# Kernel tuning notes

Hardware: AMD Instinct MI355X
Metric: run time of the kernel (lower is better)

## Reference

```python
import jax, jax.numpy as jnp
from jax import lax
import numpy as np

BLANK = 0
NEG = -1e30  # finite stand-in for -inf to keep gradients well-defined


def setup_inputs() -> dict:
    key = jax.random.key(0)
    k1, k2, k3, k4 = jax.random.split(key, 4)
    B, T, U, V = 16, 200, 100, 512
    acts = jax.random.normal(k1, (B, T, U + 1, V), dtype=jnp.float32)
    labels = jax.random.randint(k2, (B, U), 1, V, dtype=jnp.int32)  # non-blank labels
    act_lens = jax.random.randint(k3, (B,), 150, T + 1, dtype=jnp.int32)
    label_lens = jax.random.randint(k4, (B,), 50, U + 1, dtype=jnp.int32)
    return {"acts": acts, "labels": labels, "act_lens": act_lens, "label_lens": label_lens}


def _rnnt_costs(acts, labels, act_lens, label_lens):
    """Per-utterance RNN-T negative log-likelihood via forward DP over the
    (time, label) lattice. acts: (B,T,U+1,V) raw logits."""
    B, T, U1, V = acts.shape
    lp = jax.nn.log_softmax(acts, axis=-1)          # (B,T,U1,V)
    blank_lp = lp[..., BLANK]                        # (B,T,U1)
    # emit_lp[b,t,u] = lp[b,t,u,labels[b,u]]; pad labels to U1 (last col masked)
    labels_pad = jnp.pad(labels, ((0, 0), (0, 1)))   # (B,U1)
    idx = jnp.broadcast_to(labels_pad[:, None, :, None], (B, T, U1, 1))
    emit_lp = jnp.take_along_axis(lp, idx, axis=-1)[..., 0]  # (B,T,U1)
    # disallow emitting beyond each utterance's label length
    valid_u = jnp.arange(U1)[None, :] < label_lens[:, None]   # (B,U1)
    emit_lp = jnp.where(valid_u[:, None, :], emit_lp, NEG)

    # alpha[t,u]: log-prob of emitting first u labels using t frames
    # row t=0: alpha[0,u] = sum_{k<u} emit[0,k]
    row0 = jnp.concatenate(
        [jnp.zeros((B, 1), acts.dtype), jnp.cumsum(emit_lp[:, 0, :-1], axis=1)], axis=1)

    def t_step(prev_row, xs):
        blank_tm1, emit_t = xs                       # each (B,U1)
        noemit = prev_row + blank_tm1                # came from (t-1,u) via blank
        a0 = noemit[:, 0]

        def u_step(a_prev, xs_u):
            ne_u, em_um1 = xs_u                      # (B,), (B,)
            a_new = jnp.logaddexp(ne_u, a_prev + em_um1)
            return a_new, a_new

        _, rest = lax.scan(u_step, a0, (noemit[:, 1:].T, emit_t[:, :-1].T))  # (U1-1,B)
        row = jnp.concatenate([a0[:, None], rest.T], axis=1)  # (B,U1)
        return row, row

    xs = (jnp.moveaxis(blank_lp[:, :-1], 1, 0),      # blank at t-1, t=1..T-1
          jnp.moveaxis(emit_lp[:, 1:], 1, 0))        # emit at t,    t=1..T-1
    _, rows = lax.scan(t_step, row0, xs)             # (T-1,B,U1)
    alpha = jnp.concatenate([row0[None], rows], axis=0)  # (T,B,U1)
    alpha = jnp.moveaxis(alpha, 0, 1)                # (B,T,U1)

    b_idx = jnp.arange(B)
    t_idx = act_lens - 1
    u_idx = label_lens
    ll = alpha[b_idx, t_idx, u_idx] + blank_lp[b_idx, t_idx, u_idx]
    return -ll                                       # (B,)


def reference(acts, labels, act_lens, label_lens):
    costs = _rnnt_costs(acts, labels, act_lens, label_lens)
    B = acts.shape[0]
    # reduction='mean' in this impl: sum over batch then divide by batch size
    return (jnp.sum(costs) / B)[None]                # shape (1,)
```

## Files before the change

kernel.cpp:

```cpp
#include <hip/hip_runtime.h>
#include <math.h>

#define NEG -1e30f

constexpr int B  = 16;
constexpr int T  = 200;
constexpr int U  = 100;
constexpr int U1 = 101;
constexpr int V  = 512;
constexpr int NDIAG = T + U1 - 1;

__device__ __forceinline__ float logaddexpf_(float a, float b) {
    float mx = fmaxf(a, b);
    float mn = fminf(a, b);
    return mx + log1pf(__expf(mn - mx));
}

__global__ void lse_extract_kernel(const float* __restrict__ acts,
                                   const int*   __restrict__ labels,
                                   const int*   __restrict__ label_lens,
                                   float* __restrict__ blankD,
                                   float* __restrict__ emitD) {
    const int nrows = B * T * U1;
    int gid   = blockIdx.x * blockDim.x + threadIdx.x;
    int wave  = gid >> 6;
    int lane  = threadIdx.x & 63;
    int nwaves = (gridDim.x * blockDim.x) >> 6;
    for (int row = wave; row < nrows; row += nwaves) {
        const float*  p  = acts + (size_t)row * V;
        const float4* p4 = (const float4*)p;
        float4 x0 = p4[lane * 2];
        float4 x1 = p4[lane * 2 + 1];
        float m = fmaxf(fmaxf(fmaxf(x0.x, x0.y), fmaxf(x0.z, x0.w)),
                        fmaxf(fmaxf(x1.x, x1.y), fmaxf(x1.z, x1.w)));
        #pragma unroll
        for (int off = 32; off; off >>= 1) m = fmaxf(m, __shfl_xor(m, off, 64));
        float s = __expf(x0.x - m) + __expf(x0.y - m) + __expf(x0.z - m) + __expf(x0.w - m)
                + __expf(x1.x - m) + __expf(x1.y - m) + __expf(x1.z - m) + __expf(x1.w - m);
        #pragma unroll
        for (int off = 32; off; off >>= 1) s += __shfl_xor(s, off, 64);
        float lse = m + __logf(s);
        if (lane == 0) {
            int u  = row % U1;
            int bt = row / U1;
            int t  = bt % T;
            int b  = bt / T;
            size_t dpos = ((size_t)b * NDIAG + (t + u)) * U1 + u;
            blankD[dpos] = x0.x - lse;
            float e = NEG;
            if (u < label_lens[b]) {
                int lab = labels[b * U + u];
                e = p[lab] - lse;
            }
            emitD[dpos] = e;
        }
    }
}

__global__ void __launch_bounds__(128) dp_kernel(const float* __restrict__ blankD,
                                                 const float* __restrict__ emitD,
                                                 const int*   __restrict__ act_lens,
                                                 const int*   __restrict__ label_lens,
                                                 float* __restrict__ costs) {
    int b = blockIdx.x;
    int u = threadIdx.x;
    const float* bl = blankD + (size_t)b * NDIAG * U1;
    const float* em = emitD  + (size_t)b * NDIAG * U1;
    int t_end = act_lens[b] - 1;
    int u_end = label_lens[b];
    __shared__ float diag[2][U1];
    if (u == 0) diag[0][0] = 0.0f;
    float bl_r = 0.0f, em_r = 0.0f;
    if (u < U1) {
        bl_r = bl[u];
        if (u >= 1) em_r = em[u - 1];
    }
    __syncthreads();
    for (int d = 1; d < NDIAG; ++d) {
        const float* prev = diag[(d - 1) & 1];
        float*       cur  = diag[d & 1];
        int  t = d - u;
        bool active = (u < U1) && (t >= 0) && (t < T);
        float val = 0.0f;
        if (active) {
            if (t == 0)            val = prev[u - 1] + em_r;
            else if (u == 0)       val = prev[0] + bl_r;
            else                   val = logaddexpf_(prev[u] + bl_r,
                                                     prev[u - 1] + em_r);
        }
        float bl_n = 0.0f, em_n = 0.0f;
        if (u < U1 && d < NDIAG - 1) {
            bl_n = bl[d * U1 + u];
            if (u >= 1) em_n = em[d * U1 + u - 1];
        }
        if (active) {
            cur[u] = val;
            if (t == t_end && u == u_end)
                costs[b] = -(val + bl[d * U1 + u]);
        }
        bl_r = bl_n;
        em_r = em_n;
        __syncthreads();
    }
}

__global__ void finalize_kernel(const float* __restrict__ costs, float* __restrict__ out) {
    int lane = threadIdx.x;
    float v = (lane < B) ? costs[lane] : 0.0f;
    #pragma unroll
    for (int off = 8; off; off >>= 1) v += __shfl_xor(v, off, 64);
    if (lane == 0) out[0] = v * (1.0f / (float)B);
}

extern "C" void kernel_launch(void* const* d_in, const int* in_sizes, int n_in,
                              void* d_out, int out_size, void* d_ws, size_t ws_size,
                              hipStream_t stream) {
    const float* acts       = (const float*)d_in[0];
    const int*   labels     = (const int*)d_in[1];
    const int*   act_lens   = (const int*)d_in[2];
    const int*   label_lens = (const int*)d_in[3];
    float* out = (float*)d_out;

    float* blankD = (float*)d_ws;
    float* emitD  = blankD + (size_t)B * NDIAG * U1;
    float* costs  = emitD  + (size_t)B * NDIAG * U1;

    lse_extract_kernel<<<4096, 256, 0, stream>>>(acts, labels, label_lens, blankD, emitD);
    dp_kernel<<<B, 128, 0, stream>>>(blankD, emitD, act_lens, label_lens, costs);
    finalize_kernel<<<1, 64, 0, stream>>>(costs, out);
}
```

Measured before the change: 1.068 ms.

## Skip lattice rows beyond sequence lengths and run DP in one wave

The log-softmax extraction kernel now skips rows where t is at or past act_len or u is past label_len, writing NEG sentinels instead of reading the 512-wide logits row. This avoids reading and reducing acts that cannot affect the final cost. The diagonal DP kernel is rewritten to use a single 64-lane wave in which each lane holds two lattice cells. Neighbour values are passed with shuffles instead of shared memory and block barriers, and the blank/emit loads are prefetched four diagonals ahead in registers. The result relies on the skipped cells never feeding the cell read at (act_len-1, label_len).

New measurement: 1.084 ms. Within noise of the previous version (+1.5%).

```diff
diff --git a/kernel.cpp b/kernel.cpp
--- a/kernel.cpp
+++ b/kernel.cpp
@@ -18,6 +18,7 @@
 
 __global__ void lse_extract_kernel(const float* __restrict__ acts,
                                    const int*   __restrict__ labels,
+                                   const int*   __restrict__ act_lens,
                                    const int*   __restrict__ label_lens,
                                    float* __restrict__ blankD,
                                    float* __restrict__ emitD) {
@@ -26,7 +27,20 @@
     int wave  = gid >> 6;
     int lane  = threadIdx.x & 63;
     int nwaves = (gridDim.x * blockDim.x) >> 6;
+    int al_v = (lane < B) ? act_lens[lane]   : 0;
+    int ll_v = (lane < B) ? label_lens[lane] : 0;
     for (int row = wave; row < nrows; row += nwaves) {
+        int u  = row % U1;
+        int bt = row / U1;
+        int t  = bt % T;
+        int b  = bt / T;
+        int al = __shfl(al_v, b, 64);
+        int ll = __shfl(ll_v, b, 64);
+        size_t dpos = ((size_t)b * NDIAG + (t + u)) * U1 + u;
+        if (t >= al || u > ll) {
+            if (lane == 0) { blankD[dpos] = NEG; emitD[dpos] = NEG; }
+            continue;
+        }
         const float*  p  = acts + (size_t)row * V;
         const float4* p4 = (const float4*)p;
         float4 x0 = p4[lane * 2];
@@ -41,14 +55,9 @@
         for (int off = 32; off; off >>= 1) s += __shfl_xor(s, off, 64);
         float lse = m + __logf(s);
         if (lane == 0) {
-            int u  = row % U1;
-            int bt = row / U1;
-            int t  = bt % T;
-            int b  = bt / T;
-            size_t dpos = ((size_t)b * NDIAG + (t + u)) * U1 + u;
             blankD[dpos] = x0.x - lse;
             float e = NEG;
-            if (u < label_lens[b]) {
+            if (u < ll) {
                 int lab = labels[b * U + u];
                 e = p[lab] - lse;
             }
@@ -57,50 +66,71 @@
     }
 }
 
-__global__ void __launch_bounds__(128) dp_kernel(const float* __restrict__ blankD,
-                                                 const float* __restrict__ emitD,
-                                                 const int*   __restrict__ act_lens,
-                                                 const int*   __restrict__ label_lens,
-                                                 float* __restrict__ costs) {
+__global__ void __launch_bounds__(64) dp_kernel(const float* __restrict__ blankD,
+                                                const float* __restrict__ emitD,
+                                                const int*   __restrict__ act_lens,
+                                                const int*   __restrict__ label_lens,
+                                                float* __restrict__ costs) {
     int b = blockIdx.x;
-    int u = threadIdx.x;
+    int l = threadIdx.x;
     const float* bl = blankD + (size_t)b * NDIAG * U1;
     const float* em = emitD  + (size_t)b * NDIAG * U1;
     int t_end = act_lens[b] - 1;
     int u_end = label_lens[b];
-    __shared__ float diag[2][U1];
-    if (u == 0) diag[0][0] = 0.0f;
-    float bl_r = 0.0f, em_r = 0.0f;
-    if (u < U1) {
-        bl_r = bl[u];
-        if (u >= 1) em_r = em[u - 1];
+    int dF    = t_end + u_end;
+    float blF = bl[(size_t)dF * U1 + u_end];
+
+    float A0 = (l == 0) ? 0.0f : NEG;
+    float A1 = NEG;
+
+    constexpr int PF = 4;
+    float pbl0[PF], pem0[PF], pbl1[PF], pem1[PF];
+    #pragma unroll
+    for (int s = 0; s < PF; ++s) {
+        int base = s * U1;
+        pbl0[s] = bl[base + l];
+        pem0[s] = (l >= 1)  ? em[base + l - 1]  : NEG;
+        pbl1[s] = (l <= 36) ? bl[base + l + 64] : NEG;
+        pem1[s] = (l <= 37) ? em[base + l + 63] : NEG;
     }
-    __syncthreads();
-    for (int d = 1; d < NDIAG; ++d) {
-        const float* prev = diag[(d - 1) & 1];
-        float*       cur  = diag[d & 1];
-        int  t = d - u;
-        bool active = (u < U1) && (t >= 0) && (t < T);
-        float val = 0.0f;
-        if (active) {
-            if (t == 0)            val = prev[u - 1] + em_r;
-            else if (u == 0)       val = prev[0] + bl_r;
-            else                   val = logaddexpf_(prev[u] + bl_r,
-                                                     prev[u - 1] + em_r);
+
+    #pragma unroll 4
+    for (int d = 1; d <= 300; ++d) {
+        int slot = (d - 1) & 3;
+        float bl0 = pbl0[slot], em0 = pem0[slot];
+        float bl1 = pbl1[slot], em1 = pem1[slot];
+
+        float A0m1 = __shfl_up(A0, 1, 64);
+        float A1m1 = __shfl_up(A1, 1, 64);
+        float a63  = __shfl(A0, 63, 64);
+        if (l == 0) A1m1 = a63;
+
+        int t0 = d - l;
+        int t1 = t0 - 64;
+
+        float v0;
+        if (l == 0)        v0 = A0 + bl0;
+        else if (t0 == 0)  v0 = A0m1 + em0;
+        else               v0 = logaddexpf_(A0 + bl0, A0m1 + em0);
+        if (t0 >= 0 && t0 < T) A0 = v0;
+
+        float v1;
+        if (t1 == 0)       v1 = A1m1 + em1;
+        else               v1 = logaddexpf_(A1 + bl1, A1m1 + em1);
+        if (l <= 36 && t1 >= 0 && t1 < T) A1 = v1;
+
+        if (d == dF) {
+            if (u_end < 64) { if (l == u_end)      costs[b] = -(A0 + blF); }
+            else            { if (l == u_end - 64) costs[b] = -(A1 + blF); }
         }
-        float bl_n = 0.0f, em_n = 0.0f;
-        if (u < U1 && d < NDIAG - 1) {
-            bl_n = bl[d * U1 + u];
-            if (u >= 1) em_n = em[d * U1 + u - 1];
+
+        if (d + PF <= 300) {
+            int base = (d + PF - 1) * U1;
+            pbl0[slot] = bl[base + l];
+            pem0[slot] = (l >= 1)  ? em[base + l - 1]  : NEG;
+            pbl1[slot] = (l <= 36) ? bl[base + l + 64] : NEG;
+            pem1[slot] = (l <= 37) ? em[base + l + 63] : NEG;
         }
-        if (active) {
-            cur[u] = val;
-            if (t == t_end && u == u_end)
-                costs[b] = -(val + bl[d * U1 + u]);
-        }
-        bl_r = bl_n;
-        em_r = em_n;
-        __syncthreads();
     }
 }
 
@@ -125,7 +155,7 @@
     float* emitD  = blankD + (size_t)B * NDIAG * U1;
     float* costs  = emitD  + (size_t)B * NDIAG * U1;
 
-    lse_extract_kernel<<<4096, 256, 0, stream>>>(acts, labels, label_lens, blankD, emitD);
-    dp_kernel<<<B, 128, 0, stream>>>(blankD, emitD, act_lens, label_lens, costs);
+    lse_extract_kernel<<<4096, 256, 0, stream>>>(acts, labels, act_lens, label_lens, blankD, emitD);
+    dp_kernel<<<B, 64, 0, stream>>>(blankD, emitD, act_lens, label_lens, costs);
     finalize_kernel<<<1, 64, 0, stream>>>(costs, out);
 }
```
